# Kernel tuning notes

Measured on AMD Instinct MI355X. Metric: run time of the kernel, lower is better.

The kernel has to match this reference:

```python
import jax, jax.numpy as jnp
import numpy as np

B, S, DM = 4, 4096, 1024
H, DH = 16, 64          # num_attention_heads, attention_head_size
K = 128                 # Linformer projection dim (k_dims)


def setup_inputs() -> dict:
    key = jax.random.key(0)
    ks = jax.random.split(key, 9)
    s = 1.0 / np.sqrt(DM)
    return {
        "hidden_states": jax.random.normal(ks[0], (B, S, DM), jnp.float32),
        "Wq": jax.random.normal(ks[1], (DM, DM), jnp.float32) * s,
        "bq": jax.random.normal(ks[2], (DM,), jnp.float32) * 0.02,
        "Wk": jax.random.normal(ks[3], (DM, DM), jnp.float32) * s,
        "bk": jax.random.normal(ks[4], (DM,), jnp.float32) * 0.02,
        "Wv": jax.random.normal(ks[5], (DM, DM), jnp.float32) * s,
        "bv": jax.random.normal(ks[6], (DM,), jnp.float32) * 0.02,
        # E, D: [k_dims, max_input_len], init randn/sqrt(k_dims) as in torch module
        "E": jax.random.normal(ks[7], (K, S), jnp.float32) / np.sqrt(K),
        "D": jax.random.normal(ks[8], (K, S), jnp.float32) / np.sqrt(K),
    }


def reference(hidden_states, Wq, bq, Wk, bk, Wv, bv, E, D):
    b, s, _ = hidden_states.shape

    def heads(x):  # [b,s,DM] -> [b,H,s,DH]
        return x.reshape(b, s, H, DH).transpose(0, 2, 1, 3)

    # torch Linear: y = x @ W.T + b
    q = heads(hidden_states @ Wq.T + bq)   # [b,H,s,DH]
    k = heads(hidden_states @ Wk.T + bk)   # [b,H,s,DH]
    v = heads(hidden_states @ Wv.T + bv)   # [b,H,s,DH]

    # Linformer low-rank projection along the sequence axis
    pk = jnp.einsum('ks,bhsd->bhkd', E[:, :s], k)  # [b,H,K,DH]
    pv = jnp.einsum('ks,bhsd->bhkd', D[:, :s], v)  # [b,H,K,DH]

    scores = jnp.einsum('bhsd,bhkd->bhsk', q, pk) / np.sqrt(DH).astype(np.float32)
    probs = jax.nn.softmax(scores, axis=-1)        # [b,H,s,K]
    ctx = jnp.einsum('bhsk,bhkd->bhsd', probs, pv) # [b,H,s,DH]
    return ctx.transpose(0, 2, 1, 3).reshape(b, s, H * DH)
```

## Files before the change

kernel.cpp:

```cpp
#include <hip/hip_runtime.h>
#include <hip/hip_bf16.h>
#include <stdint.h>


typedef __attribute__((ext_vector_type(8))) _Float16 f16x8;
typedef __attribute__((ext_vector_type(4))) _Float16 f16x4;
typedef __attribute__((ext_vector_type(4))) float    f32x4;

__device__ __forceinline__ f32x4 mfma16(f16x8 a, f16x8 b, f32x4 c) {
    return __builtin_amdgcn_mfma_f32_16x16x32_f16(a, b, c, 0, 0, 0);
}

__device__ __forceinline__ void gload16(const void* g, void* l) {
    __builtin_amdgcn_global_load_lds(
        (const __attribute__((address_space(1))) void*)g,
        (__attribute__((address_space(3))) void*)l, 16, 0, 0);
}

__global__ __launch_bounds__(256) void prep_all(
    const float* __restrict__ hs, _Float16* __restrict__ hsB,
    const float* __restrict__ Wq, _Float16* __restrict__ WqB,
    const float* __restrict__ Wk, _Float16* __restrict__ WkH, _Float16* __restrict__ WkL,
    const float* __restrict__ Wv, _Float16* __restrict__ WvH, _Float16* __restrict__ WvL,
    const float* __restrict__ Em, _Float16* __restrict__ EB,
    const float* __restrict__ Dm, _Float16* __restrict__ DB,
    float* __restrict__ sE, float* __restrict__ sD) {
    __shared__ float red[256];
    const int blk = blockIdx.x, tid = threadIdx.x;

    if (blk < 2048) {
        int i = blk * 256 + tid;
        for (; i < 4194304; i += 2048 * 256) {
            f32x4 v = reinterpret_cast<const f32x4*>(hs)[i];
            f16x4 o;
#pragma unroll
            for (int j = 0; j < 4; ++j) o[j] = (_Float16)v[j];
            reinterpret_cast<f16x4*>(hsB)[i] = o;
        }
    } else if (blk < 2304) {
        int i = (blk - 2048) * 256 + tid;
        for (; i < 262144; i += 256 * 256) {
            f32x4 v = reinterpret_cast<const f32x4*>(Wq)[i];
            f16x4 o;
#pragma unroll
            for (int j = 0; j < 4; ++j) o[j] = (_Float16)v[j];
            reinterpret_cast<f16x4*>(WqB)[i] = o;
        }
    } else if (blk < 2816) {
        const int sect = (blk - 2304) >> 8;
        const float* in = sect ? Wv : Wk;
        _Float16* hi = sect ? WvH : WkH;
        _Float16* lo = sect ? WvL : WkL;
        int i = ((blk - 2304) & 255) * 256 + tid;
        for (; i < 262144; i += 256 * 256) {
            f32x4 v = reinterpret_cast<const f32x4*>(in)[i];
            f16x4 h, l;
#pragma unroll
            for (int j = 0; j < 4; ++j) {
                _Float16 hb = (_Float16)v[j];
                h[j] = hb;
                l[j] = (_Float16)(v[j] - (float)hb);
            }
            reinterpret_cast<f16x4*>(hi)[i] = h;
            reinterpret_cast<f16x4*>(lo)[i] = l;
        }
    } else if (blk < 3072) {
        const int sect = (blk - 2816) >> 7;
        const float* in = sect ? Dm : Em;
        _Float16* out = sect ? DB : EB;
        int i = ((blk - 2816) & 127) * 256 + tid;
        for (; i < 131072; i += 128 * 256) {
            f32x4 v = reinterpret_cast<const f32x4*>(in)[i];
            f16x4 o;
#pragma unroll
            for (int j = 0; j < 4; ++j) o[j] = (_Float16)v[j];
            reinterpret_cast<f16x4*>(out)[i] = o;
        }
    } else {
        const int rb = blk - 3072;
        const float* src = (rb < 128) ? Em : Dm;
        float* dst = (rb < 128) ? sE : sD;
        const int row = rb & 127;
        float s = 0.f;
        for (int i = tid; i < 4096; i += 256) s += src[(size_t)row * 4096 + i];
        red[tid] = s;
        __syncthreads();
        for (int off = 128; off > 0; off >>= 1) {
            if (tid < off) red[tid] += red[tid + off];
            __syncthreads();
        }
        if (tid == 0) dst[row] = red[0];
    }
}

__global__ __launch_bounds__(256, 4) void gemm_q_f16(
    const _Float16* __restrict__ A, const _Float16* __restrict__ B,
    const float* __restrict__ bias, _Float16* __restrict__ Q) {
    const int Kd = 1024, N = 1024, NT = 16;
    __shared__ _Float16 Asm[128 * 64];
    __shared__ _Float16 Bsm[128 * 64];
    const int tid = threadIdx.x, lane = tid & 63, wave = tid >> 6;
    const int l15 = lane & 15, lg = lane >> 4;
    const int row0 = blockIdx.x * 128, col0 = blockIdx.y * 128;
    const int wr = (wave >> 1) * 64, wc = (wave & 1) * 64;
    f32x4 acc[4][4];
#pragma unroll
    for (int m = 0; m < 4; ++m)
#pragma unroll
        for (int n = 0; n < 4; ++n) acc[m][n] = (f32x4)0.0f;

    const _Float16* aSrc[4];
    const _Float16* bSrc[4];
    int ub[4];
#pragma unroll
    for (int it = 0; it < 4; ++it) {
        int u = it * 256 + tid;
        int r = u >> 3, c = u & 7;
        int sc = (c ^ (r & 7)) * 8;
        aSrc[it] = A + (size_t)(row0 + r) * Kd + sc;
        bSrc[it] = B + (size_t)(col0 + r) * Kd + sc;
        ub[it] = it * 256 + wave * 64;
    }

#pragma unroll 1
    for (int t = 0; t < NT; ++t) {
        __syncthreads();
        const int k0 = t * 64;
#pragma unroll
        for (int it = 0; it < 4; ++it)
            gload16(aSrc[it] + k0, &Asm[ub[it] * 8]);
#pragma unroll
        for (int it = 0; it < 4; ++it)
            gload16(bSrc[it] + k0, &Bsm[ub[it] * 8]);
        asm volatile("s_waitcnt vmcnt(0)" ::: "memory");
        __syncthreads();
#pragma unroll
        for (int kk = 0; kk < 2; ++kk) {
            const int ksw = ((kk * 4 + lg) ^ (l15 & 7)) * 8;
            f16x8 af[4], bfr[4];
#pragma unroll
            for (int m = 0; m < 4; ++m)
                af[m] = *reinterpret_cast<const f16x8*>(
                    &Asm[(wr + m * 16 + l15) * 64 + ksw]);
#pragma unroll
            for (int n = 0; n < 4; ++n)
                bfr[n] = *reinterpret_cast<const f16x8*>(
                    &Bsm[(wc + n * 16 + l15) * 64 + ksw]);
#pragma unroll
            for (int m = 0; m < 4; ++m)
#pragma unroll
                for (int n = 0; n < 4; ++n) acc[m][n] = mfma16(af[m], bfr[n], acc[m][n]);
        }
    }
#pragma unroll
    for (int m = 0; m < 4; ++m)
#pragma unroll
        for (int n = 0; n < 4; ++n) {
            int colg = col0 + wc + n * 16 + l15;
            float bi = bias[colg];
#pragma unroll
            for (int r = 0; r < 4; ++r) {
                int rowg = row0 + wr + m * 16 + lg * 4 + r;
                Q[(size_t)rowg * N + colg] = (_Float16)(acc[m][n][r] + bi);
            }
        }
}

__global__ __launch_bounds__(256) void eproj2(const _Float16* __restrict__ EB,
                                              const _Float16* __restrict__ DB,
                                              const _Float16* __restrict__ X,
                                              float* __restrict__ EHf,
                                              float* __restrict__ DHf) {
    __shared__ _Float16 Ea[128 * 72];
    __shared__ _Float16 BT[128 * 72];
    const int tid = threadIdx.x, lane = tid & 63, wave = tid >> 6;
    const int l15 = lane & 15, lg = lane >> 4;
    const int sc = blockIdx.x;
    const int n0 = blockIdx.y * 128;
    const int bb = blockIdx.z & 3;
    const _Float16* Emat = (blockIdx.z >> 2) ? DB : EB;
    float* Of = (blockIdx.z >> 2) ? DHf : EHf;
    const int wr = (wave >> 1) * 64, wc = (wave & 1) * 64;
    const int nb = tid & 31, sb = tid >> 5;
    f32x4 acc[4][4];
#pragma unroll
    for (int m = 0; m < 4; ++m)
#pragma unroll
        for (int n = 0; n < 4; ++n) acc[m][n] = (f32x4)0.0f;

    for (int ks = 0; ks < 1024; ks += 64) {
        const int s0 = sc * 1024 + ks;
        __syncthreads();
#pragma unroll
        for (int i = 0; i < 4; ++i) {
            int u = tid + 256 * i;
            int r = u >> 3, c8 = (u & 7) * 8;
            *reinterpret_cast<f16x8*>(&Ea[r * 72 + c8]) =
                *reinterpret_cast<const f16x8*>(Emat + (size_t)r * 4096 + s0 + c8);
        }
        {
            f16x4 rr[8];
#pragma unroll
            for (int i = 0; i < 8; ++i)
                rr[i] = *reinterpret_cast<const f16x4*>(
                    X + (size_t)(bb * 4096 + s0 + sb * 8 + i) * 1024 + n0 + nb * 4);
#pragma unroll
            for (int j = 0; j < 4; ++j) {
                f16x8 w;
#pragma unroll
                for (int i = 0; i < 8; ++i) w[i] = rr[i][j];
                *reinterpret_cast<f16x8*>(&BT[(nb * 4 + j) * 72 + sb * 8]) = w;
            }
        }
        __syncthreads();
#pragma unroll
        for (int kk = 0; kk < 2; ++kk) {
            f16x8 af[4], bfr[4];
#pragma unroll
            for (int m = 0; m < 4; ++m)
                af[m] = *reinterpret_cast<const f16x8*>(
                    &Ea[(wr + m * 16 + l15) * 72 + kk * 32 + lg * 8]);
#pragma unroll
            for (int n = 0; n < 4; ++n)
                bfr[n] = *reinterpret_cast<const f16x8*>(
                    &BT[(wc + n * 16 + l15) * 72 + kk * 32 + lg * 8]);
#pragma unroll
            for (int m = 0; m < 4; ++m)
#pragma unroll
                for (int n = 0; n < 4; ++n) acc[m][n] = mfma16(af[m], bfr[n], acc[m][n]);
        }
    }
#pragma unroll
    for (int m = 0; m < 4; ++m)
#pragma unroll
        for (int n = 0; n < 4; ++n)
#pragma unroll
            for (int r = 0; r < 4; ++r)
                atomicAdd(&Of[(size_t)(bb * 128 + wr + m * 16 + lg * 4 + r) * 1024 +
                              n0 + wc + n * 16 + l15],
                          acc[m][n][r]);
}

__global__ __launch_bounds__(256) void gemm_split2(
    const float* __restrict__ A0, const _Float16* __restrict__ Bh0,
    const _Float16* __restrict__ Bl0, const float* __restrict__ bias0,
    const float* __restrict__ rs0, _Float16* __restrict__ PKH,
    const float* __restrict__ A1, const _Float16* __restrict__ Bh1,
    const _Float16* __restrict__ Bl1, const float* __restrict__ bias1,
    const float* __restrict__ rs1, _Float16* __restrict__ PVT) {
    const int Kd = 1024;
    const float* A = blockIdx.z ? A1 : A0;
    const _Float16* Bh = blockIdx.z ? Bh1 : Bh0;
    const _Float16* Bl = blockIdx.z ? Bl1 : Bl0;
    const float* bias = blockIdx.z ? bias1 : bias0;
    const float* rowscale = blockIdx.z ? rs1 : rs0;
    __shared__ _Float16 Ah[64 * 40], Al[64 * 40], Bhs[64 * 40], Bls[64 * 40];
    const int tid = threadIdx.x, lane = tid & 63, wave = tid >> 6;
    const int l15 = lane & 15, lg = lane >> 4;
    const int row0 = blockIdx.x * 64, col0 = blockIdx.y * 64;
    const int wr = (wave >> 1) * 32, wc = (wave & 1) * 32;
    f32x4 acc[2][2];
#pragma unroll
    for (int m = 0; m < 2; ++m)
#pragma unroll
        for (int n = 0; n < 2; ++n) acc[m][n] = (f32x4)0.0f;

    const int r = tid >> 2, c8 = (tid & 3) * 8;
    for (int k0 = 0; k0 < Kd; k0 += 32) {
        __syncthreads();
        {
            const float* src = A + (size_t)(row0 + r) * Kd + k0 + c8;
            f32x4 v0 = *reinterpret_cast<const f32x4*>(src);
            f32x4 v1 = *reinterpret_cast<const f32x4*>(src + 4);
            f16x8 h8, l8;
#pragma unroll
            for (int j = 0; j < 4; ++j) {
                _Float16 hb = (_Float16)v0[j];
                h8[j] = hb; l8[j] = (_Float16)(v0[j] - (float)hb);
            }
#pragma unroll
            for (int j = 0; j < 4; ++j) {
                _Float16 hb = (_Float16)v1[j];
                h8[4 + j] = hb; l8[4 + j] = (_Float16)(v1[j] - (float)hb);
            }
            *reinterpret_cast<f16x8*>(&Ah[r * 40 + c8]) = h8;
            *reinterpret_cast<f16x8*>(&Al[r * 40 + c8]) = l8;
            *reinterpret_cast<f16x8*>(&Bhs[r * 40 + c8]) =
                *reinterpret_cast<const f16x8*>(Bh + (size_t)(col0 + r) * Kd + k0 + c8);
            *reinterpret_cast<f16x8*>(&Bls[r * 40 + c8]) =
                *reinterpret_cast<const f16x8*>(Bl + (size_t)(col0 + r) * Kd + k0 + c8);
        }
        __syncthreads();
        f16x8 ah[2], al[2], bh[2], bl[2];
#pragma unroll
        for (int m = 0; m < 2; ++m) {
            ah[m] = *reinterpret_cast<const f16x8*>(&Ah[(wr + m * 16 + l15) * 40 + lg * 8]);
            al[m] = *reinterpret_cast<const f16x8*>(&Al[(wr + m * 16 + l15) * 40 + lg * 8]);
        }
#pragma unroll
        for (int n = 0; n < 2; ++n) {
            bh[n] = *reinterpret_cast<const f16x8*>(&Bhs[(wc + n * 16 + l15) * 40 + lg * 8]);
            bl[n] = *reinterpret_cast<const f16x8*>(&Bls[(wc + n * 16 + l15) * 40 + lg * 8]);
        }
#pragma unroll
        for (int m = 0; m < 2; ++m)
#pragma unroll
            for (int n = 0; n < 2; ++n) {
                acc[m][n] = mfma16(ah[m], bh[n], acc[m][n]);
                acc[m][n] = mfma16(al[m], bh[n], acc[m][n]);
                acc[m][n] = mfma16(ah[m], bl[n], acc[m][n]);
            }
    }
#pragma unroll
    for (int m = 0; m < 2; ++m)
#pragma unroll
        for (int n = 0; n < 2; ++n) {
            int colg = col0 + wc + n * 16 + l15;
            float bi = bias[colg];
#pragma unroll
            for (int rr2 = 0; rr2 < 4; ++rr2) {
                int rowg = row0 + wr + m * 16 + lg * 4 + rr2;
                float val = acc[m][n][rr2] + rowscale[rowg & 127] * bi;
                if (blockIdx.z == 0) {
                    PKH[(size_t)rowg * 1024 + colg] = (_Float16)(val * 0.125f);
                } else {
                    PVT[(size_t)((rowg >> 7) * 16 + (colg >> 6)) * 8192 +
                        (colg & 63) * 128 + (rowg & 127)] = (_Float16)val;
                }
            }
        }
}

__global__ __launch_bounds__(256, 4) void attn_fused(
    const _Float16* __restrict__ QH, const _Float16* __restrict__ PKH,
    const _Float16* __restrict__ PVT, float* __restrict__ Out) {
    __shared__ _Float16 smem[16384];
    const int tid = threadIdx.x, lane = tid & 63, wave = tid >> 6;
    const int l15 = lane & 15, lg = lane >> 4;
    const int st = blockIdx.x, h = blockIdx.y, bb = blockIdx.z;

    {
        const _Float16* pkh_g = PKH + (size_t)(bb * 128) * 1024 + h * 64;
        const _Float16* pvt_g = PVT + (size_t)(bb * 16 + h) * 8192;
        const int su = wave * 64 + lane;
#pragma unroll
        for (int it = 0; it < 4; ++it) {
            int u = it * 256 + su;
            int ub = it * 256 + wave * 64;
            {
                int r = u >> 3, c = u & 7;
                int sc = (c ^ (r & 7)) * 8;
                gload16(pkh_g + (size_t)r * 1024 + sc, &smem[ub * 8]);
            }
            {
                int r = u >> 4, c = u & 15;
                int sc = (c ^ (r & 7)) * 8;
                gload16(pvt_g + r * 128 + sc, &smem[8192 + ub * 8]);
            }
        }
    }
    const int srow0 = bb * 4096 + st * 128 + wave * 32;
    f16x8 qf[2][2];
#pragma unroll
    for (int m = 0; m < 2; ++m)
#pragma unroll
        for (int kk = 0; kk < 2; ++kk)
            qf[m][kk] = *reinterpret_cast<const f16x8*>(
                QH + (size_t)(srow0 + m * 16 + l15) * 1024 + h * 64 + kk * 32 + lg * 8);
    __syncthreads();

    f32x4 accT[8][2];
#pragma unroll
    for (int n = 0; n < 8; ++n)
#pragma unroll
        for (int m = 0; m < 2; ++m) accT[n][m] = (f32x4)0.0f;
#pragma unroll
    for (int kk = 0; kk < 2; ++kk)
#pragma unroll
        for (int n = 0; n < 8; ++n) {
            f16x8 pk = *reinterpret_cast<const f16x8*>(
                &smem[(n * 16 + l15) * 64 + (((kk * 4 + lg) ^ (l15 & 7)) * 8)]);
#pragma unroll
            for (int m = 0; m < 2; ++m)
                accT[n][m] = mfma16(pk, qf[m][kk], accT[n][m]);
        }
    __syncthreads();

#pragma unroll
    for (int m = 0; m < 2; ++m) {
        float v = -1e30f;
#pragma unroll
        for (int n = 0; n < 8; ++n)
#pragma unroll
            for (int r = 0; r < 4; ++r) v = fmaxf(v, accT[n][m][r]);
        v = fmaxf(v, __shfl_xor(v, 16));
        v = fmaxf(v, __shfl_xor(v, 32));
        float s = 0.f;
#pragma unroll
        for (int n = 0; n < 8; ++n)
#pragma unroll
            for (int r = 0; r < 4; ++r) {
                float e = __expf(accT[n][m][r] - v);
                accT[n][m][r] = e;
                s += e;
            }
        s += __shfl_xor(s, 16);
        s += __shfl_xor(s, 32);
        float inv = 1.0f / s;
#pragma unroll
        for (int n = 0; n < 8; ++n)
#pragma unroll
            for (int r = 0; r < 4; ++r) accT[n][m][r] *= inv;
    }

    _Float16* pw = smem + wave * 2048;
    f32x4 o[2][4];
#pragma unroll
    for (int m = 0; m < 2; ++m)
#pragma unroll
        for (int n = 0; n < 4; ++n) o[m][n] = (f32x4)0.0f;
#pragma unroll
    for (int half = 0; half < 2; ++half) {
#pragma unroll
        for (int nl = 0; nl < 4; ++nl) {
            int n = half * 4 + nl;
#pragma unroll
            for (int m = 0; m < 2; ++m) {
                int q = l15 + 16 * m;
                int kp = (nl * 8 + lg * 2) ^ ((q & 7) << 2);
                f16x4 v;
#pragma unroll
                for (int r = 0; r < 4; ++r) v[r] = (_Float16)accT[n][m][r];
                *reinterpret_cast<f16x4*>(&pw[q * 64 + kp * 2]) = v;
            }
        }
#pragma unroll
        for (int ksl = 0; ksl < 2; ++ksl) {
            f16x8 pa[2];
#pragma unroll
            for (int m = 0; m < 2; ++m) {
                int q = m * 16 + l15;
                int kpb = (ksl * 16 + lg * 4) ^ ((q & 7) << 2);
                pa[m] = *reinterpret_cast<const f16x8*>(&pw[q * 64 + kpb * 2]);
            }
            int ks = half * 2 + ksl;
#pragma unroll
            for (int n = 0; n < 4; ++n) {
                int dd = n * 16 + l15;
                f16x8 bv = *reinterpret_cast<const f16x8*>(
                    &smem[8192 + dd * 128 + (((ks * 4 + lg) ^ (dd & 7)) * 8)]);
#pragma unroll
                for (int m = 0; m < 2; ++m) o[m][n] = mfma16(pa[m], bv, o[m][n]);
            }
        }
    }

#pragma unroll
    for (int m = 0; m < 2; ++m)
#pragma unroll
        for (int n = 0; n < 4; ++n)
#pragma unroll
            for (int r = 0; r < 4; ++r) {
                int row = srow0 + m * 16 + lg * 4 + r;
                Out[(size_t)row * 1024 + h * 64 + n * 16 + l15] = o[m][n][r];
            }
}

extern "C" void kernel_launch(void* const* d_in, const int* in_sizes, int n_in,
                              void* d_out, int out_size, void* d_ws, size_t ws_size,
                              hipStream_t stream) {
    const float* hs = (const float*)d_in[0];
    const float* Wq = (const float*)d_in[1];
    const float* bq = (const float*)d_in[2];
    const float* Wk = (const float*)d_in[3];
    const float* bk = (const float*)d_in[4];
    const float* Wv = (const float*)d_in[5];
    const float* bv = (const float*)d_in[6];
    const float* Em = (const float*)d_in[7];
    const float* Dm = (const float*)d_in[8];
    float* out = (float*)d_out;
    char* ws = (char*)d_ws;

    _Float16* hsB = (_Float16*)(ws + 0);
    _Float16* WqB = (_Float16*)(ws + 33554432);
    _Float16* WkH = (_Float16*)(ws + 35651584);
    _Float16* WkL = (_Float16*)(ws + 37748736);
    _Float16* WvH = (_Float16*)(ws + 39845888);
    _Float16* WvL = (_Float16*)(ws + 41943040);
    _Float16* EB  = (_Float16*)(ws + 44040192);
    _Float16* DB  = (_Float16*)(ws + 45088768);
    float* sE  = (float*)(ws + 46137344);
    float* sD  = (float*)(ws + 46137856);
    _Float16* QHq = (_Float16*)(ws + 46138368);
    float* EHf = (float*)(ws + 113247232);
    float* DHf = (float*)(ws + 115344384);
    _Float16* PKH = (_Float16*)(ws + 117441536);
    _Float16* PVT = (_Float16*)(ws + 118490112);

    prep_all<<<3328, 256, 0, stream>>>(hs, hsB, Wq, WqB, Wk, WkH, WkL,
                                       Wv, WvH, WvL, Em, EB, Dm, DB, sE, sD);
    gemm_q_f16<<<dim3(128, 8), 256, 0, stream>>>(hsB, WqB, bq, QHq);
    hipMemsetAsync(EHf, 0, 2 * 512 * 1024 * sizeof(float), stream);
    eproj2<<<dim3(4, 8, 8), 256, 0, stream>>>(EB, DB, hsB, EHf, DHf);
    gemm_split2<<<dim3(8, 16, 2), 256, 0, stream>>>(EHf, WkH, WkL, bk, sE, PKH,
                                                    DHf, WvH, WvL, bv, sD, PVT);
    attn_fused<<<dim3(32, 16, 4), 256, 0, stream>>>(QHq, PKH, PVT, out);
}
```

Measured before the change: 151.8 us.

## Fuse Q projection GEMM into Linformer attention kernel

Merges the Q projection GEMM with the attention kernel, so each 128x128 Q tile feeds straight into scores, softmax and the PV product held in registers and LDS. This avoids writing the fp16 Q buffer to global memory and reading it back, and removes one kernel launch. In exchange, PK fragments are held in registers and PV fragments are read directly from global memory rather than staged in LDS. Launch bounds drop to 3 waves per SIMD to make room for the extra register pressure.

```diff
diff --git a/kernel.cpp b/kernel.cpp
--- a/kernel.cpp
+++ b/kernel.cpp
@@ -91,79 +91,6 @@
         }
         if (tid == 0) dst[row] = red[0];
     }
-}
-
-__global__ __launch_bounds__(256, 4) void gemm_q_f16(
-    const _Float16* __restrict__ A, const _Float16* __restrict__ B,
-    const float* __restrict__ bias, _Float16* __restrict__ Q) {
-    const int Kd = 1024, N = 1024, NT = 16;
-    __shared__ _Float16 Asm[128 * 64];
-    __shared__ _Float16 Bsm[128 * 64];
-    const int tid = threadIdx.x, lane = tid & 63, wave = tid >> 6;
-    const int l15 = lane & 15, lg = lane >> 4;
-    const int row0 = blockIdx.x * 128, col0 = blockIdx.y * 128;
-    const int wr = (wave >> 1) * 64, wc = (wave & 1) * 64;
-    f32x4 acc[4][4];
-#pragma unroll
-    for (int m = 0; m < 4; ++m)
-#pragma unroll
-        for (int n = 0; n < 4; ++n) acc[m][n] = (f32x4)0.0f;
-
-    const _Float16* aSrc[4];
-    const _Float16* bSrc[4];
-    int ub[4];
-#pragma unroll
-    for (int it = 0; it < 4; ++it) {
-        int u = it * 256 + tid;
-        int r = u >> 3, c = u & 7;
-        int sc = (c ^ (r & 7)) * 8;
-        aSrc[it] = A + (size_t)(row0 + r) * Kd + sc;
-        bSrc[it] = B + (size_t)(col0 + r) * Kd + sc;
-        ub[it] = it * 256 + wave * 64;
-    }
-
-#pragma unroll 1
-    for (int t = 0; t < NT; ++t) {
-        __syncthreads();
-        const int k0 = t * 64;
-#pragma unroll
-        for (int it = 0; it < 4; ++it)
-            gload16(aSrc[it] + k0, &Asm[ub[it] * 8]);
-#pragma unroll
-        for (int it = 0; it < 4; ++it)
-            gload16(bSrc[it] + k0, &Bsm[ub[it] * 8]);
-        asm volatile("s_waitcnt vmcnt(0)" ::: "memory");
-        __syncthreads();
-#pragma unroll
-        for (int kk = 0; kk < 2; ++kk) {
-            const int ksw = ((kk * 4 + lg) ^ (l15 & 7)) * 8;
-            f16x8 af[4], bfr[4];
-#pragma unroll
-            for (int m = 0; m < 4; ++m)
-                af[m] = *reinterpret_cast<const f16x8*>(
-                    &Asm[(wr + m * 16 + l15) * 64 + ksw]);
-#pragma unroll
-            for (int n = 0; n < 4; ++n)
-                bfr[n] = *reinterpret_cast<const f16x8*>(
-                    &Bsm[(wc + n * 16 + l15) * 64 + ksw]);
-#pragma unroll
-            for (int m = 0; m < 4; ++m)
-#pragma unroll
-                for (int n = 0; n < 4; ++n) acc[m][n] = mfma16(af[m], bfr[n], acc[m][n]);
-        }
-    }
-#pragma unroll
-    for (int m = 0; m < 4; ++m)
-#pragma unroll
-        for (int n = 0; n < 4; ++n) {
-            int colg = col0 + wc + n * 16 + l15;
-            float bi = bias[colg];
-#pragma unroll
-            for (int r = 0; r < 4; ++r) {
-                int rowg = row0 + wr + m * 16 + lg * 4 + r;
-                Q[(size_t)rowg * N + colg] = (_Float16)(acc[m][n][r] + bi);
-            }
-        }
 }
 
 __global__ __launch_bounds__(256) void eproj2(const _Float16* __restrict__ EB,
@@ -331,139 +258,191 @@
         }
 }
 
-__global__ __launch_bounds__(256, 4) void attn_fused(
-    const _Float16* __restrict__ QH, const _Float16* __restrict__ PKH,
+__global__ __launch_bounds__(256, 3) void gemm_q_attn(
+    const _Float16* __restrict__ A, const _Float16* __restrict__ B,
+    const float* __restrict__ bias, const _Float16* __restrict__ PKH,
     const _Float16* __restrict__ PVT, float* __restrict__ Out) {
+    const int Kd = 1024, NT = 16;
     __shared__ _Float16 smem[16384];
+    _Float16* Asm = smem;
+    _Float16* Bsm = smem + 8192;
     const int tid = threadIdx.x, lane = tid & 63, wave = tid >> 6;
     const int l15 = lane & 15, lg = lane >> 4;
-    const int st = blockIdx.x, h = blockIdx.y, bb = blockIdx.z;
-
-    {
-        const _Float16* pkh_g = PKH + (size_t)(bb * 128) * 1024 + h * 64;
-        const _Float16* pvt_g = PVT + (size_t)(bb * 16 + h) * 8192;
-        const int su = wave * 64 + lane;
-#pragma unroll
-        for (int it = 0; it < 4; ++it) {
-            int u = it * 256 + su;
-            int ub = it * 256 + wave * 64;
-            {
-                int r = u >> 3, c = u & 7;
-                int sc = (c ^ (r & 7)) * 8;
-                gload16(pkh_g + (size_t)r * 1024 + sc, &smem[ub * 8]);
-            }
-            {
-                int r = u >> 4, c = u & 15;
-                int sc = (c ^ (r & 7)) * 8;
-                gload16(pvt_g + r * 128 + sc, &smem[8192 + ub * 8]);
-            }
-        }
-    }
-    const int srow0 = bb * 4096 + st * 128 + wave * 32;
-    f16x8 qf[2][2];
-#pragma unroll
-    for (int m = 0; m < 2; ++m)
+    const int row0 = blockIdx.x * 128, col0 = blockIdx.y * 128;
+    const int wr = (wave >> 1) * 64, wc = (wave & 1) * 64;
+    f32x4 acc[4][4];
+#pragma unroll
+    for (int m = 0; m < 4; ++m)
+#pragma unroll
+        for (int n = 0; n < 4; ++n) acc[m][n] = (f32x4)0.0f;
+
+    const _Float16* aSrc[4];
+    const _Float16* bSrc[4];
+    int ub[4];
+#pragma unroll
+    for (int it = 0; it < 4; ++it) {
+        int u = it * 256 + tid;
+        int r = u >> 3, c = u & 7;
+        int sc = (c ^ (r & 7)) * 8;
+        aSrc[it] = A + (size_t)(row0 + r) * Kd + sc;
+        bSrc[it] = B + (size_t)(col0 + r) * Kd + sc;
+        ub[it] = it * 256 + wave * 64;
+    }
+
+#pragma unroll 1
+    for (int t = 0; t < NT; ++t) {
+        __syncthreads();
+        const int k0 = t * 64;
+#pragma unroll
+        for (int it = 0; it < 4; ++it)
+            gload16(aSrc[it] + k0, &Asm[ub[it] * 8]);
+#pragma unroll
+        for (int it = 0; it < 4; ++it)
+            gload16(bSrc[it] + k0, &Bsm[ub[it] * 8]);
+        asm volatile("s_waitcnt vmcnt(0)" ::: "memory");
+        __syncthreads();
+#pragma unroll
+        for (int kk = 0; kk < 2; ++kk) {
+            const int ksw = ((kk * 4 + lg) ^ (l15 & 7)) * 8;
+            f16x8 af[4], bfr[4];
+#pragma unroll
+            for (int m = 0; m < 4; ++m)
+                af[m] = *reinterpret_cast<const f16x8*>(
+                    &Asm[(wr + m * 16 + l15) * 64 + ksw]);
+#pragma unroll
+            for (int n = 0; n < 4; ++n)
+                bfr[n] = *reinterpret_cast<const f16x8*>(
+                    &Bsm[(wc + n * 16 + l15) * 64 + ksw]);
+#pragma unroll
+            for (int m = 0; m < 4; ++m)
+#pragma unroll
+                for (int n = 0; n < 4; ++n) acc[m][n] = mfma16(af[m], bfr[n], acc[m][n]);
+        }
+    }
+
+    const int hd = blockIdx.y * 2 + (wave & 1);
+    const int bb = blockIdx.x >> 5;
+    const _Float16* pkg = PKH + (size_t)(bb * 128) * 1024 + hd * 64;
+    const _Float16* pvg = PVT + (size_t)(bb * 16 + hd) * 8192;
+    float bi[4];
+#pragma unroll
+    for (int n = 0; n < 4; ++n) bi[n] = bias[col0 + wc + n * 16 + l15];
+
+    f16x8 pk[8][2];
+#pragma unroll
+    for (int n = 0; n < 8; ++n)
 #pragma unroll
         for (int kk = 0; kk < 2; ++kk)
-            qf[m][kk] = *reinterpret_cast<const f16x8*>(
-                QH + (size_t)(srow0 + m * 16 + l15) * 1024 + h * 64 + kk * 32 + lg * 8);
+            pk[n][kk] = *reinterpret_cast<const f16x8*>(
+                pkg + (size_t)(n * 16 + l15) * 1024 + kk * 32 + lg * 8);
+
     __syncthreads();
-
-    f32x4 accT[8][2];
-#pragma unroll
-    for (int n = 0; n < 8; ++n)
-#pragma unroll
-        for (int m = 0; m < 2; ++m) accT[n][m] = (f32x4)0.0f;
-#pragma unroll
-    for (int kk = 0; kk < 2; ++kk)
-#pragma unroll
-        for (int n = 0; n < 8; ++n) {
-            f16x8 pk = *reinterpret_cast<const f16x8*>(
-                &smem[(n * 16 + l15) * 64 + (((kk * 4 + lg) ^ (l15 & 7)) * 8)]);
-#pragma unroll
-            for (int m = 0; m < 2; ++m)
-                accT[n][m] = mfma16(pk, qf[m][kk], accT[n][m]);
-        }
-    __syncthreads();
-
-#pragma unroll
-    for (int m = 0; m < 2; ++m) {
-        float v = -1e30f;
+    _Float16* qs = smem + wave * 4096;
+
+#pragma unroll
+    for (int rh = 0; rh < 2; ++rh) {
+#pragma unroll
+        for (int mi = 0; mi < 2; ++mi)
+#pragma unroll
+            for (int n = 0; n < 4; ++n)
+#pragma unroll
+                for (int r = 0; r < 4; ++r)
+                    qs[(mi * 16 + lg * 4 + r) * 72 + n * 16 + l15] =
+                        (_Float16)(acc[rh * 2 + mi][n][r] + bi[n]);
+        f16x8 qB[2][2];
+#pragma unroll
+        for (int mh = 0; mh < 2; ++mh)
+#pragma unroll
+            for (int kk = 0; kk < 2; ++kk)
+                qB[mh][kk] = *reinterpret_cast<const f16x8*>(
+                    &qs[(mh * 16 + l15) * 72 + kk * 32 + lg * 8]);
+
+        f32x4 accT[8][2];
 #pragma unroll
         for (int n = 0; n < 8; ++n)
 #pragma unroll
-            for (int r = 0; r < 4; ++r) v = fmaxf(v, accT[n][m][r]);
-        v = fmaxf(v, __shfl_xor(v, 16));
-        v = fmaxf(v, __shfl_xor(v, 32));
-        float s = 0.f;
-#pragma unroll
-        for (int n = 0; n < 8; ++n)
-#pragma unroll
-            for (int r = 0; r < 4; ++r) {
-                float e = __expf(accT[n][m][r] - v);
-                accT[n][m][r] = e;
-                s += e;
-            }
-        s += __shfl_xor(s, 16);
-        s += __shfl_xor(s, 32);
-        float inv = 1.0f / s;
-#pragma unroll
-        for (int n = 0; n < 8; ++n)
-#pragma unroll
-            for (int r = 0; r < 4; ++r) accT[n][m][r] *= inv;
-    }
-
-    _Float16* pw = smem + wave * 2048;
-    f32x4 o[2][4];
-#pragma unroll
-    for (int m = 0; m < 2; ++m)
-#pragma unroll
-        for (int n = 0; n < 4; ++n) o[m][n] = (f32x4)0.0f;
-#pragma unroll
-    for (int half = 0; half < 2; ++half) {
-#pragma unroll
-        for (int nl = 0; nl < 4; ++nl) {
-            int n = half * 4 + nl;
-#pragma unroll
-            for (int m = 0; m < 2; ++m) {
-                int q = l15 + 16 * m;
-                int kp = (nl * 8 + lg * 2) ^ ((q & 7) << 2);
-                f16x4 v;
-#pragma unroll
-                for (int r = 0; r < 4; ++r) v[r] = (_Float16)accT[n][m][r];
-                *reinterpret_cast<f16x4*>(&pw[q * 64 + kp * 2]) = v;
-            }
-        }
-#pragma unroll
-        for (int ksl = 0; ksl < 2; ++ksl) {
-            f16x8 pa[2];
-#pragma unroll
-            for (int m = 0; m < 2; ++m) {
-                int q = m * 16 + l15;
-                int kpb = (ksl * 16 + lg * 4) ^ ((q & 7) << 2);
-                pa[m] = *reinterpret_cast<const f16x8*>(&pw[q * 64 + kpb * 2]);
-            }
-            int ks = half * 2 + ksl;
-#pragma unroll
-            for (int n = 0; n < 4; ++n) {
-                int dd = n * 16 + l15;
-                f16x8 bv = *reinterpret_cast<const f16x8*>(
-                    &smem[8192 + dd * 128 + (((ks * 4 + lg) ^ (dd & 7)) * 8)]);
-#pragma unroll
-                for (int m = 0; m < 2; ++m) o[m][n] = mfma16(pa[m], bv, o[m][n]);
-            }
-        }
-    }
-
-#pragma unroll
-    for (int m = 0; m < 2; ++m)
-#pragma unroll
-        for (int n = 0; n < 4; ++n)
-#pragma unroll
-            for (int r = 0; r < 4; ++r) {
-                int row = srow0 + m * 16 + lg * 4 + r;
-                Out[(size_t)row * 1024 + h * 64 + n * 16 + l15] = o[m][n][r];
-            }
+            for (int mh = 0; mh < 2; ++mh) accT[n][mh] = (f32x4)0.0f;
+#pragma unroll
+        for (int kk = 0; kk < 2; ++kk)
+#pragma unroll
+            for (int n = 0; n < 8; ++n)
+#pragma unroll
+                for (int mh = 0; mh < 2; ++mh)
+                    accT[n][mh] = mfma16(pk[n][kk], qB[mh][kk], accT[n][mh]);
+
+#pragma unroll
+        for (int mh = 0; mh < 2; ++mh) {
+            float v = -1e30f;
+#pragma unroll
+            for (int n = 0; n < 8; ++n)
+#pragma unroll
+                for (int r = 0; r < 4; ++r) v = fmaxf(v, accT[n][mh][r]);
+            v = fmaxf(v, __shfl_xor(v, 16));
+            v = fmaxf(v, __shfl_xor(v, 32));
+            float s = 0.f;
+#pragma unroll
+            for (int n = 0; n < 8; ++n)
+#pragma unroll
+                for (int r = 0; r < 4; ++r) {
+                    float e = __expf(accT[n][mh][r] - v);
+                    accT[n][mh][r] = e;
+                    s += e;
+                }
+            s += __shfl_xor(s, 16);
+            s += __shfl_xor(s, 32);
+            float inv = 1.0f / s;
+#pragma unroll
+            for (int n = 0; n < 8; ++n)
+#pragma unroll
+                for (int r = 0; r < 4; ++r) accT[n][mh][r] *= inv;
+        }
+
+        f32x4 o[2][4];
+#pragma unroll
+        for (int mh = 0; mh < 2; ++mh)
+#pragma unroll
+            for (int n = 0; n < 4; ++n) o[mh][n] = (f32x4)0.0f;
+#pragma unroll
+        for (int kh = 0; kh < 2; ++kh) {
+#pragma unroll
+            for (int nl = 0; nl < 4; ++nl)
+#pragma unroll
+                for (int mh = 0; mh < 2; ++mh) {
+                    f16x4 v;
+#pragma unroll
+                    for (int r = 0; r < 4; ++r) v[r] = (_Float16)accT[kh * 4 + nl][mh][r];
+                    *reinterpret_cast<f16x4*>(
+                        &qs[(mh * 16 + l15) * 72 + nl * 16 + lg * 4]) = v;
+                }
+#pragma unroll
+            for (int ksl = 0; ksl < 2; ++ksl) {
+                f16x8 pa[2];
+#pragma unroll
+                for (int mh = 0; mh < 2; ++mh)
+                    pa[mh] = *reinterpret_cast<const f16x8*>(
+                        &qs[(mh * 16 + l15) * 72 + ksl * 32 + lg * 8]);
+#pragma unroll
+                for (int n = 0; n < 4; ++n) {
+                    f16x8 bv = *reinterpret_cast<const f16x8*>(
+                        pvg + (size_t)(n * 16 + l15) * 128 +
+                        (kh * 2 + ksl) * 32 + lg * 8);
+#pragma unroll
+                    for (int mh = 0; mh < 2; ++mh)
+                        o[mh][n] = mfma16(pa[mh], bv, o[mh][n]);
+                }
+            }
+        }
+
+#pragma unroll
+        for (int mh = 0; mh < 2; ++mh)
+#pragma unroll
+            for (int n = 0; n < 4; ++n)
+#pragma unroll
+                for (int r = 0; r < 4; ++r) {
+                    int row = row0 + wr + rh * 32 + mh * 16 + lg * 4 + r;
+                    Out[(size_t)row * 1024 + hd * 64 + n * 16 + l15] = o[mh][n][r];
+                }
+    }
 }
 
 extern "C" void kernel_launch(void* const* d_in, const int* in_sizes, int n_in,
@@ -491,7 +470,6 @@
     _Float16* DB  = (_Float16*)(ws + 45088768);
     float* sE  = (float*)(ws + 46137344);
     float* sD  = (float*)(ws + 46137856);
-    _Float16* QHq = (_Float16*)(ws + 46138368);
     float* EHf = (float*)(ws + 113247232);
     float* DHf = (float*)(ws + 115344384);
     _Float16* PKH = (_Float16*)(ws + 117441536);
@@ -499,10 +477,9 @@
 
     prep_all<<<3328, 256, 0, stream>>>(hs, hsB, Wq, WqB, Wk, WkH, WkL,
                                        Wv, WvH, WvL, Em, EB, Dm, DB, sE, sD);
-    gemm_q_f16<<<dim3(128, 8), 256, 0, stream>>>(hsB, WqB, bq, QHq);
     hipMemsetAsync(EHf, 0, 2 * 512 * 1024 * sizeof(float), stream);
     eproj2<<<dim3(4, 8, 8), 256, 0, stream>>>(EB, DB, hsB, EHf, DHf);
     gemm_split2<<<dim3(8, 16, 2), 256, 0, stream>>>(EHf, WkH, WkL, bk, sE, PKH,
                                                     DHf, WvH, WvL, bv, sD, PVT);
-    attn_fused<<<dim3(32, 16, 4), 256, 0, stream>>>(QHq, PKH, PVT, out);
-}
+    gemm_q_attn<<<dim3(128, 8), 256, 0, stream>>>(hsB, WqB, bq, PKH, PVT, out);
+}
```

Result: slower. 178.6 us (+17.6%).
